# Optimization experiments

Measured on AMD Instinct MI355X. Metric: run time of the kernel, lower is better.

## Reference

```python
import math
import jax, jax.numpy as jnp
import numpy as np

B, L, CIN, COUT = 128, 100, 55, 55
D, H, DFF, MODES = 512, 8, 512, 32
E = D // H
KERNELS = (12, 24)
NK = len(KERNELS)


def _pos_emb(length, d):
    pos = np.arange(length)[:, None].astype(np.float32)
    div = np.exp(np.arange(0, d, 2).astype(np.float32) * (-math.log(10000.0) / d))
    pe = np.zeros((length, d), dtype=np.float32)
    pe[:, 0::2] = np.sin(pos * div)
    pe[:, 1::2] = np.cos(pos * div)
    return jnp.asarray(pe)


def _circ_conv3(x, W):
    # Conv1d(kernel=3, padding=1, padding_mode='circular', bias=False); x:(B,L,C) W:(O,C,3)
    n = x.shape[1]
    xp = jnp.concatenate([x[:, -1:], x, x[:, :1]], axis=1)
    return (jnp.einsum('blc,oc->blo', xp[:, 0:n], W[:, :, 0]) +
            jnp.einsum('blc,oc->blo', xp[:, 1:n + 1], W[:, :, 1]) +
            jnp.einsum('blc,oc->blo', xp[:, 2:n + 2], W[:, :, 2]))


def _moving_avg(x, k):
    # replicate-pad then length-preserving mean filter (Autoformer moving_avg)
    front = jnp.repeat(x[:, :1], (k - 1) // 2, axis=1)
    end = jnp.repeat(x[:, -1:], k // 2, axis=1)
    xp = jnp.concatenate([front, x, end], axis=1)
    c = jnp.cumsum(xp, axis=1)
    c = jnp.concatenate([jnp.zeros_like(c[:, :1]), c], axis=1)
    return (c[:, k:] - c[:, :-k]) / float(k)


def _decomp(x, w, b):
    # series_decomp_multi with learned softmax mixing (Linear(1, NK))
    means = jnp.stack([_moving_avg(x, k) for k in KERNELS], axis=-1)  # (B,L,D,NK)
    mix = jax.nn.softmax(x[..., None] * w + b, axis=-1)
    mean = jnp.sum(means * mix, axis=-1)
    return x - mean, mean


def _my_layernorm(x, g, b):
    mu = x.mean(-1, keepdims=True)
    var = ((x - mu) ** 2).mean(-1, keepdims=True)
    xh = (x - mu) / jnp.sqrt(var + 1e-5) * g + b
    return xh - xh.mean(axis=1, keepdims=True)


def _fourier_block(q, Wc):
    # q:(B,L,H,E) -> rfft over L, per-mode complex GEMM with Wc:(H,E,E,MODES), irfft
    x = jnp.transpose(q, (0, 2, 3, 1))  # (B,H,E,L)
    xf = jnp.fft.rfft(x, axis=-1)
    sel = jnp.einsum('bhem,heom->bhom', xf[..., :MODES], Wc)
    nfreq = x.shape[-1] // 2 + 1
    out_ft = jnp.zeros(sel.shape[:-1] + (nfreq,), sel.dtype).at[..., :MODES].set(sel)
    out = jnp.fft.irfft(out_ft, n=x.shape[-1], axis=-1)
    return jnp.transpose(out, (0, 3, 1, 2))  # (B,L,H,E)


def _fourier_cross(q, k, Wc):
    # FourierCrossAttention: frequency-domain q*k attention with tanh activation, values = k
    xq = jnp.transpose(q, (0, 2, 3, 1))
    xk = jnp.transpose(k, (0, 2, 3, 1))
    qf = jnp.fft.rfft(xq, axis=-1)[..., :MODES]
    kf = jnp.fft.rfft(xk, axis=-1)[..., :MODES]
    qk = jnp.tanh(jnp.einsum('bhex,bhey->bhxy', qf, kf))
    qkv = jnp.einsum('bhxy,bhey->bhex', qk, kf)
    w = jnp.einsum('bhex,heox->bhox', qkv, Wc)
    nfreq = xq.shape[-1] // 2 + 1
    out_ft = jnp.zeros(w.shape[:-1] + (nfreq,), w.dtype).at[..., :MODES].set(w)
    out = jnp.fft.irfft(out_ft / float(D * D), n=xq.shape[-1], axis=-1)
    return jnp.transpose(out, (0, 3, 1, 2))


def _heads(x, W, b):
    y = x @ W.T + b
    return y.reshape(y.shape[0], y.shape[1], H, E)


def _gelu(x):
    return jax.nn.gelu(x, approximate=False)


def _forward(x, emb_enc_w, emb_dec_w, enc_proj_w, enc_proj_b, enc_sig_w, enc_sig_b,
             enc_four_wr, enc_four_wi, enc_ffn_w1, enc_ffn_w2, enc_dcmp_w, enc_dcmp_b,
             enc_norm_g, enc_norm_b, dec_proj_w, dec_proj_b, dec_four_wr, dec_four_wi,
             crs_proj_w, crs_proj_b, crs_four_wr, crs_four_wi, dec_ffn_w1, dec_ffn_w2,
             dec_dcmp_w, dec_dcmp_b, dec_trend_w, dec_norm_g, dec_norm_b,
             out_proj_w, out_proj_b):
    b, n, _ = x.shape
    dist = jnp.abs(jnp.arange(n)[:, None] - jnp.arange(n)[None, :]).astype(x.dtype)
    # seasonal-trend init decomposition
    trend_init = jnp.broadcast_to(x.mean(axis=1, keepdims=True), x.shape)
    seasonal_init = x - trend_init
    pe = _pos_emb(n, D)
    enc_four = enc_four_wr + 1j * enc_four_wi
    enc = _circ_conv3(x, emb_enc_w) + pe
    series_l, prior_l, sigma_l = [], [], []
    for i in range(enc_proj_w.shape[0]):  # e_layers (structurally distinct params)
        Wp, bp = enc_proj_w[i], enc_proj_b[i]
        q = _heads(enc, Wp[0], bp[0])
        k = _heads(enc, Wp[1], bp[1])
        v = _heads(enc, Wp[2], bp[2])  # projected but unused by FourierBlock (faithful)
        attn_out = _fourier_block(q, enc_four).reshape(b, n, D) @ Wp[3].T + bp[3]
        # Anomaly-Transformer association: series = softmax(QK^T/sqrt(E)), prior = Gaussian kernel
        scores = jnp.einsum('blhe,bshe->bhls', q, k) / math.sqrt(E)
        series = jax.nn.softmax(scores, axis=-1)
        sig = jnp.transpose(enc @ enc_sig_w[i].T + enc_sig_b[i], (0, 2, 1))  # (B,H,L)
        sig = jnp.power(3.0, jax.nn.sigmoid(5.0 * sig) + 1e-5) - 1.0
        prior = jnp.exp(-dist ** 2 / (2.0 * sig[..., None] ** 2)) / (math.sqrt(2.0 * math.pi) * sig[..., None])
        series_l.append(series); prior_l.append(prior); sigma_l.append(sig)
        h = enc + attn_out
        h, _ = _decomp(h, enc_dcmp_w[i, 0], enc_dcmp_b[i, 0])
        y = _gelu(h @ enc_ffn_w1[i].T) @ enc_ffn_w2[i].T
        enc, _ = _decomp(h + y, enc_dcmp_w[i, 1], enc_dcmp_b[i, 1])
    enc = _my_layernorm(enc, enc_norm_g, enc_norm_b)

    # decoder (d_layers = 1)
    dec = _circ_conv3(seasonal_init, emb_dec_w) + pe
    dec_four = dec_four_wr + 1j * dec_four_wi
    crs_four = crs_four_wr + 1j * crs_four_wi
    q = _heads(dec, dec_proj_w[0], dec_proj_b[0])
    sa = _fourier_block(q, dec_four).reshape(b, n, D) @ dec_proj_w[3].T + dec_proj_b[3]
    h = dec + sa
    h, t1 = _decomp(h, dec_dcmp_w[0], dec_dcmp_b[0])
    qc = _heads(h, crs_proj_w[0], crs_proj_b[0])
    kc = _heads(enc, crs_proj_w[1], crs_proj_b[1])
    ca = _fourier_cross(qc, kc, crs_four).reshape(b, n, D) @ crs_proj_w[3].T + crs_proj_b[3]
    h = h + ca
    h, t2 = _decomp(h, dec_dcmp_w[1], dec_dcmp_b[1])
    y = _gelu(h @ dec_ffn_w1.T) @ dec_ffn_w2.T
    h, t3 = _decomp(h + y, dec_dcmp_w[2], dec_dcmp_b[2])
    residual_trend = _circ_conv3(t1 + t2 + t3, dec_trend_w)  # (B,L,COUT)
    trend = trend_init + residual_trend
    h = _my_layernorm(h, dec_norm_g, dec_norm_b)
    seasonal = h @ out_proj_w.T + out_proj_b
    dec_out = trend + seasonal
    return dec_out, jnp.stack(series_l), jnp.stack(prior_l), jnp.stack(sigma_l)


def setup_inputs() -> dict:
    key = jax.random.key(0)
    ks = iter(jax.random.split(key, 64))

    def rn(shape, s=0.02):
        return s * jax.random.normal(next(ks), shape, dtype=jnp.float32)

    return dict(
        x=jax.random.normal(next(ks), (B, L, CIN), dtype=jnp.float32),
        emb_enc_w=rn((D, CIN, 3)), emb_dec_w=rn((D, CIN, 3)),
        enc_proj_w=rn((2, 4, D, D)), enc_proj_b=jnp.zeros((2, 4, D), jnp.float32),
        enc_sig_w=rn((2, H, D)), enc_sig_b=jnp.zeros((2, H), jnp.float32),
        enc_four_wr=rn((H, E, E, MODES)), enc_four_wi=rn((H, E, E, MODES)),
        enc_ffn_w1=rn((2, DFF, D)), enc_ffn_w2=rn((2, D, DFF)),
        enc_dcmp_w=rn((2, 2, NK), 1.0), enc_dcmp_b=jnp.zeros((2, 2, NK), jnp.float32),
        enc_norm_g=jnp.ones((D,), jnp.float32), enc_norm_b=jnp.zeros((D,), jnp.float32),
        dec_proj_w=rn((4, D, D)), dec_proj_b=jnp.zeros((4, D), jnp.float32),
        dec_four_wr=rn((H, E, E, MODES)), dec_four_wi=rn((H, E, E, MODES)),
        crs_proj_w=rn((4, D, D)), crs_proj_b=jnp.zeros((4, D), jnp.float32),
        crs_four_wr=rn((H, E, E, MODES)), crs_four_wi=rn((H, E, E, MODES)),
        dec_ffn_w1=rn((DFF, D)), dec_ffn_w2=rn((D, DFF)),
        dec_dcmp_w=rn((3, NK), 1.0), dec_dcmp_b=jnp.zeros((3, NK), jnp.float32),
        dec_trend_w=rn((COUT, D, 3)),
        dec_norm_g=jnp.ones((D,), jnp.float32), dec_norm_b=jnp.zeros((D,), jnp.float32),
        out_proj_w=rn((COUT, D)), out_proj_b=jnp.zeros((COUT,), jnp.float32),
    )


def reference(x, emb_enc_w, emb_dec_w, enc_proj_w, enc_proj_b, enc_sig_w, enc_sig_b,
              enc_four_wr, enc_four_wi, enc_ffn_w1, enc_ffn_w2, enc_dcmp_w, enc_dcmp_b,
              enc_norm_g, enc_norm_b, dec_proj_w, dec_proj_b, dec_four_wr, dec_four_wi,
              crs_proj_w, crs_proj_b, crs_four_wr, crs_four_wi, dec_ffn_w1, dec_ffn_w2,
              dec_dcmp_w, dec_dcmp_b, dec_trend_w, dec_norm_g, dec_norm_b,
              out_proj_w, out_proj_b):
    return _forward(x, emb_enc_w, emb_dec_w, enc_proj_w, enc_proj_b, enc_sig_w, enc_sig_b,
                    enc_four_wr, enc_four_wi, enc_ffn_w1, enc_ffn_w2, enc_dcmp_w, enc_dcmp_b,
                    enc_norm_g, enc_norm_b, dec_proj_w, dec_proj_b, dec_four_wr, dec_four_wi,
                    crs_proj_w, crs_proj_b, crs_four_wr, crs_four_wi, dec_ffn_w1, dec_ffn_w2,
                    dec_dcmp_w, dec_dcmp_b, dec_trend_w, dec_norm_g, dec_norm_b,
                    out_proj_w, out_proj_b)
```

## Files before the change

### kernel.cpp

```cpp
#include <hip/hip_runtime.h>
#include <hip/hip_bf16.h>
#include <cmath>

constexpr int B = 128, L = 100, CIN = 55, COUT = 55;
constexpr int D = 512, H = 8, DFF = 512, MODES = 32, E = 64;
constexpr int NK = 2;
constexpr int M_ROWS = B * L;
constexpr int KEMB = 192;
constexpr size_t BLD  = (size_t)B * L * D;
constexpr size_t BHEM = (size_t)B * H * E * MODES;
constexpr size_t BHLL = (size_t)B * H * L * L;
constexpr float INV_SQRT_2PI = 0.3989422804014327f;

static inline int cdiv(int a, int b) { return (a + b - 1) / b; }

typedef short shortx8 __attribute__((ext_vector_type(8)));
typedef float f32x4 __attribute__((ext_vector_type(4)));

__device__ inline unsigned short f2bf(float f)
{
    unsigned int u = __float_as_uint(f);
    unsigned int r = (u + 0x7FFFu + ((u >> 16) & 1u)) >> 16;
    return (unsigned short)r;
}
__device__ inline unsigned short f2bf_n(float f)
{
    union { __hip_bfloat16 h; unsigned short u; } cv;
    cv.h = __float2bfloat16(f);
    return cv.u;
}
__device__ inline float bf2f(unsigned short u)
{
    union { unsigned int i; float f; } c;
    c.i = (unsigned int)u << 16;
    return c.f;
}

__global__ void init_consts(float* __restrict__ pe)
{
    int idx = blockIdx.x * 256 + threadIdx.x;
    if (idx < L * D) {
        int l = idx / D, d = idx % D;
        int i2 = d & ~1;
        float div = expf((float)i2 * (-logf(10000.f) / (float)D));
        float ang = (float)l * div;
        pe[idx] = (d & 1) ? cosf(ang) : sinf(ang);
    }
}

__global__ void init_tw(unsigned short* __restrict__ twf, unsigned short* __restrict__ twi)
{
    int idx = blockIdx.x * 256 + threadIdx.x;
    if (idx >= 64 * 128) return;
    {
        int mp = idx / 128, t = idx % 128;
        float v = 0.f;
        if (t < L) {
            if (mp < 32) v = cosf(2.f * 3.14159265358979323846f * (float)mp * (float)t / (float)L);
            else v = -sinf(2.f * 3.14159265358979323846f * (float)(mp - 32) * (float)t / (float)L);
        }
        twf[idx] = f2bf(v);
    }
    {
        int t = idx / 64, mp = idx % 64;
        float v = 0.f;
        if (t < L) {
            if (mp == 0) v = 1.f;
            else if (mp < 32) v = 2.f * cosf(2.f * 3.14159265358979323846f * (float)mp * (float)t / (float)L);
            else if (mp == 32) v = 0.f;
            else v = -2.f * sinf(2.f * 3.14159265358979323846f * (float)(mp - 32) * (float)t / (float)L);
        }
        twi[idx] = f2bf(v);
    }
}

__global__ void xmean_kernel(const float* __restrict__ x, float* __restrict__ xm)
{
    int idx = blockIdx.x * 256 + threadIdx.x;
    if (idx >= B * CIN) return;
    int b = idx / CIN, c = idx % CIN;
    float s = 0.f;
    for (int l = 0; l < L; ++l) s += x[((size_t)b * L + l) * CIN + c];
    xm[idx] = s * (1.f / (float)L);
}

__global__ void to_bf16(const float* __restrict__ src, unsigned short* __restrict__ dst, int n4)
{
    int i = blockIdx.x * 256 + threadIdx.x;
    if (i >= n4) return;
    float4 v = *(const float4*)&src[(size_t)i * 4];
    ushort4 h;
    h.x = f2bf(v.x); h.y = f2bf(v.y); h.z = f2bf(v.z); h.w = f2bf(v.w);
    *(ushort4*)&dst[(size_t)i * 4] = h;
}

__global__ void pad_rows_bf(const float* __restrict__ src, unsigned short* __restrict__ dst,
                            int rows_src, int rows_dst, int k_src, int k_dst)
{
    int idx = blockIdx.x * 256 + threadIdx.x;
    if (idx >= rows_dst * k_dst) return;
    int r = idx / k_dst, k = idx % k_dst;
    dst[idx] = (r < rows_src && k < k_src) ? f2bf(src[(size_t)r * k_src + k]) : (unsigned short)0;
}

__global__ void pad_trend_w2_bf(const float* __restrict__ src, unsigned short* __restrict__ dst)
{
    int idx = blockIdx.x * 256 + threadIdx.x;
    if (idx >= 192 * D) return;
    int n = idx / D, d = idx % D;
    int j = n / 64, o = n % 64;
    dst[idx] = (o < COUT) ? f2bf(src[(size_t)o * (D * 3) + d * 3 + j]) : (unsigned short)0;
}

__global__ __launch_bounds__(256) void transpose_w(const float* __restrict__ wr, const float* __restrict__ wi,
                                                   float2* __restrict__ wt)
{
    int h = blockIdx.x / E, e = blockIdx.x % E;
    __shared__ float tr[64][33], ti[64][33];
    for (int i = threadIdx.x; i < E * MODES; i += 256) {
        int o = i / MODES, m = i % MODES;
        size_t s = (((size_t)h * E + e) * E + o) * MODES + m;
        tr[o][m] = wr[s]; ti[o][m] = wi[s];
    }
    __syncthreads();
    for (int i = threadIdx.x; i < MODES * E; i += 256) {
        int m = i / E, o = i % E;
        wt[(((size_t)h * MODES + m) * E + e) * E + o] = make_float2(tr[o][m], ti[o][m]);
    }
}

__global__ void im2col_emb(const float* __restrict__ x, const float* __restrict__ xmean,
                           unsigned short* __restrict__ A2)
{
    int idx = blockIdx.x * 256 + threadIdx.x;
    if (idx >= M_ROWS * KEMB) return;
    int k = idx % KEMB, m = idx / KEMB;
    float v = 0.f;
    if (k < CIN * 3) {
        int c = k / 3, j = k % 3;
        int l = m % L, b = m / L;
        int ls = l + j - 1; ls = (ls + L) % L;
        v = x[((size_t)b * L + ls) * CIN + c];
        if (xmean) v -= xmean[(size_t)b * CIN + c];
    }
    A2[idx] = f2bf(v);
}

template<int BN>
__global__ __launch_bounds__(256) void gemm_mfma(const unsigned short* __restrict__ A,
                                                 const unsigned short* __restrict__ Wb,
                                                 const float* __restrict__ bias, const float* __restrict__ pe,
                                                 float* __restrict__ C, unsigned short* __restrict__ Cb,
                                                 int Nout, int K, int act, int accum)
{
    constexpr int NI = BN / 32;
    constexpr int BI = BN / 64;
    __shared__ unsigned short As[2][128][40];
    __shared__ unsigned short Bs[2][BN][40];
    int tid = threadIdx.x;
    int row0 = blockIdx.y * 128, col0 = blockIdx.x * BN;
    int wid = tid >> 6, lane = tid & 63;
    int wm = wid >> 1, wn = wid & 1;
    int lrow = lane & 15, kg = lane >> 4;
    int ar = tid >> 2, ac8 = (tid & 3) * 8;
    f32x4 acc[4][NI] = {};
    shortx8 rah[2], rbh[BI];

    auto loadG = [&](int k0) {
#pragma unroll
        for (int p = 0; p < 2; ++p)
            rah[p] = *(const shortx8*)&A[(size_t)(row0 + p * 64 + ar) * K + k0 + ac8];
#pragma unroll
        for (int p = 0; p < BI; ++p)
            rbh[p] = *(const shortx8*)&Wb[(size_t)(col0 + p * 64 + ar) * K + k0 + ac8];
    };
    auto storeLDS = [&](int buf) {
#pragma unroll
        for (int p = 0; p < 2; ++p)
            *(shortx8*)&As[buf][p * 64 + ar][ac8] = rah[p];
#pragma unroll
        for (int p = 0; p < BI; ++p)
            *(shortx8*)&Bs[buf][p * 64 + ar][ac8] = rbh[p];
    };

    int nk = K >> 5;
    loadG(0);
    storeLDS(0);
    if (nk > 1) loadG(32);
    __syncthreads();
    int cur = 0;
    for (int s = 0; s < nk; ++s) {
        if (s + 1 < nk) {
            storeLDS(cur ^ 1);
            if (s + 2 < nk) loadG((s + 2) << 5);
        }
        shortx8 av[4], bv[NI];
#pragma unroll
        for (int mi = 0; mi < 4; ++mi)
            av[mi] = *(const shortx8*)&As[cur][wm * 64 + mi * 16 + lrow][kg * 8];
#pragma unroll
        for (int ni = 0; ni < NI; ++ni)
            bv[ni] = *(const shortx8*)&Bs[cur][wn * (BN / 2) + ni * 16 + lrow][kg * 8];
#pragma unroll
        for (int mi = 0; mi < 4; ++mi)
#pragma unroll
            for (int ni = 0; ni < NI; ++ni)
                acc[mi][ni] = __builtin_amdgcn_mfma_f32_16x16x32_bf16(av[mi], bv[ni], acc[mi][ni], 0, 0, 0);
        if (s + 1 < nk) __syncthreads();
        cur ^= 1;
    }
#pragma unroll
    for (int mi = 0; mi < 4; ++mi) {
#pragma unroll
        for (int ni = 0; ni < NI; ++ni) {
            int col = col0 + wn * (BN / 2) + ni * 16 + lrow;
            if (col >= Nout) continue;
#pragma unroll
            for (int r = 0; r < 4; ++r) {
                int row = row0 + wm * 64 + mi * 16 + kg * 4 + r;
                float v = acc[mi][ni][r];
                if (bias) v += bias[col];
                if (pe) v += pe[(size_t)(row % L) * Nout + col];
                if (act) v = 0.5f * v * (1.f + erff(v * 0.70710678118654752f));
                size_t o = (size_t)row * Nout + col;
                if (Cb) Cb[o] = f2bf_n(v);
                else if (accum) C[o] += v;
                else C[o] = v;
            }
        }
    }
}

__global__ __launch_bounds__(256) void scores_softmax(const unsigned short* __restrict__ QK,
                                                      float* __restrict__ out)
{
    int bh = blockIdx.x, b = bh / H, h = bh % H;
    int pass = blockIdx.y;
    __shared__ unsigned short Ks[112][72];
    __shared__ unsigned short Qs[64][72];
    int tid = threadIdx.x;
    int srow = tid >> 4, sc4 = (tid & 15) * 4;
#pragma unroll
    for (int i = 0; i < 7; ++i) {
        int r = i * 16 + srow;
        ushort4 hh = {0, 0, 0, 0};
        if (r < L) hh = *(const ushort4*)&QK[((size_t)b * L + r) * 1024 + 512 + h * E + sc4];
        *(ushort4*)&Ks[r][sc4] = hh;
    }
#pragma unroll
    for (int i = 0; i < 4; ++i) {
        int r = i * 16 + srow;
        int gr = pass * 64 + r;
        ushort4 hh = {0, 0, 0, 0};
        if (gr < L) hh = *(const ushort4*)&QK[((size_t)b * L + gr) * 1024 + h * E + sc4];
        *(ushort4*)&Qs[r][sc4] = hh;
    }
    __syncthreads();
    int wid = tid >> 6, lane = tid & 63;
    int lrow = lane & 15, kg = lane >> 4;
    f32x4 acc[7] = {};
#pragma unroll
    for (int ks = 0; ks < 2; ++ks) {
        shortx8 aq = *(const shortx8*)&Qs[wid * 16 + lrow][ks * 32 + kg * 8];
#pragma unroll
        for (int tj = 0; tj < 7; ++tj) {
            shortx8 bk = *(const shortx8*)&Ks[tj * 16 + lrow][ks * 32 + kg * 8];
            acc[tj] = __builtin_amdgcn_mfma_f32_16x16x32_bf16(aq, bk, acc[tj], 0, 0, 0);
        }
    }
    float mx[4] = {-1e30f, -1e30f, -1e30f, -1e30f};
#pragma unroll
    for (int tj = 0; tj < 7; ++tj) {
        bool valid = (tj * 16 + lrow) < L;
#pragma unroll
        for (int r = 0; r < 4; ++r) {
            float v = acc[tj][r] * 0.125f;
            acc[tj][r] = valid ? v : -1e30f;
            if (valid) mx[r] = fmaxf(mx[r], v);
        }
    }
#pragma unroll
    for (int off = 1; off < 16; off <<= 1)
#pragma unroll
        for (int r = 0; r < 4; ++r) mx[r] = fmaxf(mx[r], __shfl_xor(mx[r], off));
    float sum[4] = {0.f, 0.f, 0.f, 0.f};
#pragma unroll
    for (int tj = 0; tj < 7; ++tj)
#pragma unroll
        for (int r = 0; r < 4; ++r) {
            float e = expf(acc[tj][r] - mx[r]);
            acc[tj][r] = e;
            sum[r] += e;
        }
#pragma unroll
    for (int off = 1; off < 16; off <<= 1)
#pragma unroll
        for (int r = 0; r < 4; ++r) sum[r] += __shfl_xor(sum[r], off);
    float inv[4];
#pragma unroll
    for (int r = 0; r < 4; ++r) inv[r] = 1.f / sum[r];
    float* base = out + (size_t)bh * L * L;
#pragma unroll
    for (int r = 0; r < 4; ++r) {
        int row = pass * 64 + wid * 16 + kg * 4 + r;
        if (row >= L) continue;
#pragma unroll
        for (int tj = 0; tj < 7; ++tj) {
            int col = tj * 16 + lrow;
            if (col < L) base[(size_t)row * L + col] = acc[tj][r] * inv[r];
        }
    }
}

__global__ void trend_combine(const float* __restrict__ Y, const float* __restrict__ xmean,
                              float* __restrict__ dec_out)
{
    int idx = blockIdx.x * 256 + threadIdx.x;
    if (idx >= B * L * COUT) return;
    int o = idx % COUT; int l = (idx / COUT) % L; int b = idx / (COUT * L);
    int lm = (l + L - 1) % L, lp = (l + 1) % L;
    float v = xmean[(size_t)b * CIN + o]
            + Y[((size_t)b * L + lm) * 192 + o]
            + Y[((size_t)b * L + l ) * 192 + 64 + o]
            + Y[((size_t)b * L + lp) * 192 + 128 + o];
    dec_out[idx] = v;
}

__global__ __launch_bounds__(256) void dft_mfma(const unsigned short* __restrict__ X,
                                                const unsigned short* __restrict__ twf,
                                                float2* __restrict__ xf, int stride)
{
    int b = blockIdx.x / H, h = blockIdx.x % H;
    __shared__ unsigned short Xs[64][136];
    int tid = threadIdx.x;
    for (int i = tid; i < L * E / 4; i += 256) {
        int t = i >> 4, e4 = (i & 15) * 4;
        ushort4 u = *(const ushort4*)&X[((size_t)b * L + t) * stride + h * E + e4];
        Xs[e4][t] = u.x; Xs[e4 + 1][t] = u.y; Xs[e4 + 2][t] = u.z; Xs[e4 + 3][t] = u.w;
    }
    for (int i = tid; i < 64 * 28; i += 256) {
        int e = i / 28, t = L + i % 28;
        Xs[e][t] = 0;
    }
    __syncthreads();
    int wid = tid >> 6, lane = tid & 63;
    int lrow = lane & 15, kg = lane >> 4;
    f32x4 acc[4] = {};
#pragma unroll
    for (int k0 = 0; k0 < 4; ++k0) {
        shortx8 bx = *(const shortx8*)&Xs[wid * 16 + lrow][k0 * 32 + kg * 8];
#pragma unroll
        for (int mi = 0; mi < 4; ++mi) {
            shortx8 aw = *(const shortx8*)&twf[(size_t)(mi * 16 + lrow) * 128 + k0 * 32 + kg * 8];
            acc[mi] = __builtin_amdgcn_mfma_f32_16x16x32_bf16(aw, bx, acc[mi], 0, 0, 0);
        }
    }
    int e = wid * 16 + lrow;
#pragma unroll
    for (int mi = 0; mi < 2; ++mi)
#pragma unroll
        for (int r = 0; r < 4; ++r) {
            int m = mi * 16 + kg * 4 + r;
            xf[((size_t)(h * MODES + m) * B + b) * E + e] = make_float2(acc[mi][r], acc[mi + 2][r]);
        }
}

__global__ __launch_bounds__(256) void idft_mfma(const float2* __restrict__ sel,
                                                 const unsigned short* __restrict__ twi,
                                                 unsigned short* __restrict__ out, float scale)
{
    int b = blockIdx.x / H, h = blockIdx.x % H;
    __shared__ unsigned short Ss[64][72];
    int tid = threadIdx.x;
    for (int i = tid; i < MODES * E; i += 256) {
        int m = i >> 6, o = i & 63;
        float2 v = sel[((size_t)(h * MODES + m) * B + b) * E + o];
        Ss[o][m] = f2bf_n(v.x);
        Ss[o][m + 32] = f2bf_n(v.y);
    }
    __syncthreads();
    int wid = tid >> 6, lane = tid & 63;
    int lrow = lane & 15, kg = lane >> 4;
    f32x4 acc[2][4] = {};
#pragma unroll
    for (int k0 = 0; k0 < 2; ++k0) {
        shortx8 bs[4];
#pragma unroll
        for (int ni = 0; ni < 4; ++ni)
            bs[ni] = *(const shortx8*)&Ss[ni * 16 + lrow][k0 * 32 + kg * 8];
#pragma unroll
        for (int ti = 0; ti < 2; ++ti) {
            shortx8 at = *(const shortx8*)&twi[(size_t)((wid * 2 + ti) * 16 + lrow) * 64 + k0 * 32 + kg * 8];
#pragma unroll
            for (int ni = 0; ni < 4; ++ni)
                acc[ti][ni] = __builtin_amdgcn_mfma_f32_16x16x32_bf16(at, bs[ni], acc[ti][ni], 0, 0, 0);
        }
    }
#pragma unroll
    for (int ti = 0; ti < 2; ++ti)
#pragma unroll
        for (int ni = 0; ni < 4; ++ni)
#pragma unroll
            for (int r = 0; r < 4; ++r) {
                int t = (wid * 2 + ti) * 16 + kg * 4 + r;
                if (t < L) {
                    int o = ni * 16 + lrow;
                    out[((size_t)b * L + t) * D + h * E + o] = f2bf_n(acc[ti][ni][r] * scale);
                }
            }
}

__global__ __launch_bounds__(256) void mode_gemm2(float2* __restrict__ xf, const float2* __restrict__ wt)
{
    int hm = blockIdx.x;
    int bt = blockIdx.y;
    __shared__ float2 Wc[E][E];
    __shared__ float2 Ac[32][E];
    for (int i = threadIdx.x; i < E * E; i += 256) Wc[i / E][i % E] = wt[(size_t)hm * (E * E) + i];
    for (int i = threadIdx.x; i < 32 * E; i += 256)
        Ac[i / E][i % E] = xf[((size_t)hm * B + bt * 32 + i / E) * E + i % E];
    __syncthreads();
    int o = threadIdx.x & 63, bb = threadIdx.x >> 6;
    float2 acc[8];
#pragma unroll
    for (int j = 0; j < 8; ++j) acc[j] = make_float2(0.f, 0.f);
    for (int e = 0; e < E; ++e) {
        float2 w = Wc[e][o];
#pragma unroll
        for (int j = 0; j < 8; ++j) {
            float2 a = Ac[bb * 8 + j][e];
            acc[j].x += a.x * w.x - a.y * w.y;
            acc[j].y += a.x * w.y + a.y * w.x;
        }
    }
#pragma unroll
    for (int j = 0; j < 8; ++j)
        xf[((size_t)hm * B + bt * 32 + bb * 8 + j) * E + o] = acc[j];
}

__global__ __launch_bounds__(256) void fourier_qk(const float2* __restrict__ qf, float2* __restrict__ kf)
{
    int b = blockIdx.x / H, h = blockIdx.x % H;
    __shared__ float2 qm[MODES][E + 1], km[MODES][E + 1], vm[MODES][E + 1];
    __shared__ float tr[MODES][MODES + 1], ti[MODES][MODES + 1];
    for (int i = threadIdx.x; i < MODES * E; i += 256) {
        int m = i / E, e = i % E;
        size_t idx = ((size_t)(h * MODES + m) * B + b) * E + e;
        qm[m][e] = qf[idx];
        km[m][e] = kf[idx];
    }
    __syncthreads();
    for (int i = threadIdx.x; i < MODES * MODES; i += 256) {
        int x = i / MODES, y = i % MODES;
        float re = 0.f, im = 0.f;
        for (int e = 0; e < E; ++e) {
            float2 a = qm[x][e], k2 = km[y][e];
            re += a.x * k2.x - a.y * k2.y;
            im += a.x * k2.y + a.y * k2.x;
        }
        float aa = fminf(fmaxf(2.f * re, -30.f), 30.f);
        float b2 = 2.f * im;
        float den = coshf(aa) + cosf(b2);
        tr[x][y] = sinhf(aa) / den;
        ti[x][y] = sinf(b2) / den;
    }
    __syncthreads();
    for (int i = threadIdx.x; i < MODES * E; i += 256) {
        int x = i / E, e = i % E;
        float re = 0.f, im = 0.f;
        for (int y = 0; y < MODES; ++y) {
            float ar = tr[x][y], ai = ti[x][y];
            float2 kk = km[y][e];
            re += ar * kk.x - ai * kk.y;
            im += ar * kk.y + ai * kk.x;
        }
        vm[x][e] = make_float2(re, im);
    }
    __syncthreads();
    for (int i = threadIdx.x; i < MODES * E; i += 256) {
        int m = i / E, e = i % E;
        kf[((size_t)(h * MODES + m) * B + b) * E + e] = vm[m][e];
    }
}

__global__ __launch_bounds__(256) void sigma_prior(const unsigned short* __restrict__ enc,
                                                   const float* __restrict__ w,
                                                   const float* __restrict__ bias,
                                                   float* __restrict__ sig_out, float* __restrict__ prior)
{
    __shared__ float wsh[H][D];
    for (int i = threadIdx.x; i < H * D; i += 256) wsh[i / D][i % D] = w[i];
    __syncthreads();
    int wid = threadIdx.x / 64, lane = threadIdx.x % 64;
    int row = blockIdx.x * 4 + wid;
    const unsigned short* p = enc + (size_t)row * D;
    float xv[8];
#pragma unroll
    for (int i = 0; i < 8; ++i) xv[i] = bf2f(p[lane + i * 64]);
    int b = row / L, l = row % L;
#pragma unroll
    for (int h = 0; h < H; ++h) {
        float s = 0.f;
#pragma unroll
        for (int i = 0; i < 8; ++i) s += xv[i] * wsh[h][lane + i * 64];
        for (int off = 32; off; off >>= 1) s += __shfl_xor(s, off);
        float acc = s + bias[h];
        float sg = 1.f / (1.f + expf(-5.f * acc));
        float val = expf((sg + 1e-5f) * 1.0986122886681098f) - 1.f;
        if (lane == 0) sig_out[((size_t)b * H + h) * L + l] = val;
        float inv2 = 1.f / (2.f * val * val);
        float coef = INV_SQRT_2PI / val;
        float* pr = prior + (((size_t)b * H + h) * L + l) * L;
        for (int sc = lane; sc < L; sc += 64) {
            float d = (float)abs(l - sc);
            pr[sc] = expf(-d * d * inv2) * coef;
        }
    }
}

__global__ __launch_bounds__(256) void decomp_kernel(const unsigned short* __restrict__ in1,
                                                     const unsigned short* __restrict__ in2,
                                                     const float* __restrict__ w, const float* __restrict__ bc,
                                                     unsigned short* __restrict__ res, float* __restrict__ trend,
                                                     unsigned short* __restrict__ trend16, int tmode)
{
    int b = blockIdx.x / (D / 64);
    int d0 = (blockIdx.x % (D / 64)) * 64;
    __shared__ float P[125][65];
    __shared__ float qtot[4][64];
    int tid = threadIdx.x;
    int dd = tid & 63, q = tid >> 6;
    int p0 = q * 31;
    float run = 0.f;
#pragma unroll
    for (int i = 0; i < 31; ++i) {
        int p = p0 + i;
        int j = min(max(p - 12, 0), L - 1);
        size_t g = ((size_t)b * L + j) * D + d0 + dd;
        float v = bf2f(in1[g]);
        if (in2) v += bf2f(in2[g]);
        run += v;
        P[p + 1][dd] = run;
    }
    qtot[q][dd] = run;
    if (tid < 64) P[0][dd] = 0.f;
    __syncthreads();
    if (q > 0) {
        float off = qtot[0][dd];
        if (q > 1) off += qtot[1][dd];
        if (q > 2) off += qtot[2][dd];
#pragma unroll
        for (int i = 0; i < 31; ++i)
            P[p0 + i + 1][dd] += off;
    }
    __syncthreads();
    float w0 = w[0], w1 = w[1], b0 = bc[0], b1 = bc[1];
    for (int i = tid; i < L * 64; i += 256) {
        int l = i >> 6, d2 = i & 63;
        float s12 = P[l + 19][d2] - P[l + 7][d2];
        float s24 = P[l + 25][d2] - P[l + 1][d2];
        float x = P[l + 13][d2] - P[l + 12][d2];
        float m0 = s12 * (1.f / 12.f), m1 = s24 * (1.f / 24.f);
        float z0 = x * w0 + b0, z1 = x * w1 + b1;
        float zm = fmaxf(z0, z1);
        float e0 = expf(z0 - zm), e1 = expf(z1 - zm);
        float p0f = e0 / (e0 + e1);
        float mean = m0 * p0f + m1 * (1.f - p0f);
        size_t g = ((size_t)b * L + l) * D + d0 + d2;
        res[g] = f2bf_n(x - mean);
        if (tmode == 1) trend[g] = mean;
        else if (tmode == 2) {
            float tv = trend[g] + mean;
            trend[g] = tv;
            if (trend16) trend16[g] = f2bf_n(tv);
        }
    }
}

__global__ __launch_bounds__(256) void ln_colsub(const unsigned short* __restrict__ x,
                                                 const float* __restrict__ g, const float* __restrict__ bb,
                                                 unsigned short* __restrict__ out)
{
    int b = blockIdx.x;
    __shared__ unsigned short xs[L][D];
    __shared__ float colmean[D];
    __shared__ float gs[D], bs2[D];
    int tid = threadIdx.x;
    for (int i = tid; i < L * D / 8; i += 256) {
        int l = i / 64, c8 = (i % 64) * 8;
        *(shortx8*)&xs[l][c8] = *(const shortx8*)&x[((size_t)b * L + l) * D + c8];
    }
    for (int i = tid; i < D; i += 256) { gs[i] = g[i]; bs2[i] = bb[i]; }
    __syncthreads();
    int wid = tid >> 6, lane = tid & 63;
    for (int l = wid; l < L; l += 4) {
        float v[8];
        float s = 0.f, s2 = 0.f;
#pragma unroll
        for (int i = 0; i < 8; ++i) {
            v[i] = bf2f(xs[l][lane + i * 64]);
            s += v[i]; s2 += v[i] * v[i];
        }
        for (int off = 32; off; off >>= 1) { s += __shfl_xor(s, off); s2 += __shfl_xor(s2, off); }
        float mu = s / (float)D;
        float var = s2 / (float)D - mu * mu;
        float rstd = rsqrtf(var + 1e-5f);
#pragma unroll
        for (int i = 0; i < 8; ++i) {
            int d = lane + i * 64;
            xs[l][d] = f2bf_n((v[i] - mu) * rstd * gs[d] + bs2[d]);
        }
    }
    __syncthreads();
    for (int c = tid; c < D; c += 256) {
        float s = 0.f;
        for (int l = 0; l < L; ++l) s += bf2f(xs[l][c]);
        colmean[c] = s * (1.f / (float)L);
    }
    __syncthreads();
    for (int i = tid; i < L * D; i += 256) {
        int l = i / D, c = i % D;
        out[((size_t)b * L + l) * D + c] = f2bf_n(bf2f(xs[l][c]) - colmean[c]);
    }
}

extern "C" void kernel_launch(void* const* d_in, const int* in_sizes, int n_in,
                              void* d_out, int out_size, void* d_ws, size_t ws_size,
                              hipStream_t stream)
{
    const float* x           = (const float*)d_in[0];
    const float* emb_enc_w   = (const float*)d_in[1];
    const float* emb_dec_w   = (const float*)d_in[2];
    const float* enc_proj_w  = (const float*)d_in[3];
    const float* enc_proj_b  = (const float*)d_in[4];
    const float* enc_sig_w   = (const float*)d_in[5];
    const float* enc_sig_b   = (const float*)d_in[6];
    const float* enc_four_wr = (const float*)d_in[7];
    const float* enc_four_wi = (const float*)d_in[8];
    const float* enc_ffn_w1  = (const float*)d_in[9];
    const float* enc_ffn_w2  = (const float*)d_in[10];
    const float* enc_dcmp_w  = (const float*)d_in[11];
    const float* enc_dcmp_b  = (const float*)d_in[12];
    const float* enc_norm_g  = (const float*)d_in[13];
    const float* enc_norm_b  = (const float*)d_in[14];
    const float* dec_proj_w  = (const float*)d_in[15];
    const float* dec_proj_b  = (const float*)d_in[16];
    const float* dec_four_wr = (const float*)d_in[17];
    const float* dec_four_wi = (const float*)d_in[18];
    const float* crs_proj_w  = (const float*)d_in[19];
    const float* crs_proj_b  = (const float*)d_in[20];
    const float* crs_four_wr = (const float*)d_in[21];
    const float* crs_four_wi = (const float*)d_in[22];
    const float* dec_ffn_w1  = (const float*)d_in[23];
    const float* dec_ffn_w2  = (const float*)d_in[24];
    const float* dec_dcmp_w  = (const float*)d_in[25];
    const float* dec_dcmp_b  = (const float*)d_in[26];
    const float* dec_trend_w = (const float*)d_in[27];
    const float* dec_norm_g  = (const float*)d_in[28];
    const float* dec_norm_b  = (const float*)d_in[29];
    const float* out_proj_w  = (const float*)d_in[30];
    const float* out_proj_b  = (const float*)d_in[31];

    float* ws = (float*)d_ws;
    size_t off = 0;
    float* pe    = ws + off; off += (size_t)L * D;
    float* xmean = ws + off; off += (size_t)B * CIN;
    float* bufF  = ws + off; off += BLD;
    float* tacc  = ws + off; off += BLD;
    float2* xfc  = (float2*)(ws + off); off += 2 * BHEM;
    float2* kfc  = (float2*)(ws + off); off += 2 * BHEM;
    float2* wtb  = (float2*)(ws + off); off += 2 * (size_t)H * MODES * E * E;
    unsigned short* qk16 = (unsigned short*)(ws + off); off += BLD;
    unsigned short* e16  = (unsigned short*)(ws + off); off += BLD / 2;
    unsigned short* c16  = (unsigned short*)(ws + off); off += BLD / 2;
    unsigned short* d16  = (unsigned short*)(ws + off); off += BLD / 2;
    unsigned short* h16  = (unsigned short*)(ws + off); off += BLD / 2;
    unsigned short* t16  = (unsigned short*)(ws + off); off += BLD / 2;
    unsigned short* im16 = (unsigned short*)(ws + off); off += (size_t)M_ROWS * KEMB / 2;
    unsigned short* wbf_encproj = (unsigned short*)(ws + off); off += (size_t)2 * 4 * D * D / 2;
    unsigned short* wbf_ffn1    = (unsigned short*)(ws + off); off += (size_t)2 * DFF * D / 2;
    unsigned short* wbf_ffn2    = (unsigned short*)(ws + off); off += (size_t)2 * D * DFF / 2;
    unsigned short* wbf_decproj = (unsigned short*)(ws + off); off += (size_t)4 * D * D / 2;
    unsigned short* wbf_crsproj = (unsigned short*)(ws + off); off += (size_t)4 * D * D / 2;
    unsigned short* wbf_dffn1   = (unsigned short*)(ws + off); off += (size_t)DFF * D / 2;
    unsigned short* wbf_dffn2   = (unsigned short*)(ws + off); off += (size_t)D * DFF / 2;
    unsigned short* wbf_embenc  = (unsigned short*)(ws + off); off += (size_t)D * KEMB / 2;
    unsigned short* wbf_embdec  = (unsigned short*)(ws + off); off += (size_t)D * KEMB / 2;
    unsigned short* wbf_trd     = (unsigned short*)(ws + off); off += (size_t)192 * D / 2;
    unsigned short* wbf_seas    = (unsigned short*)(ws + off); off += (size_t)64 * D / 2;
    unsigned short* twf         = (unsigned short*)(ws + off); off += (size_t)64 * 128 / 2;
    unsigned short* twi         = (unsigned short*)(ws + off); off += (size_t)128 * 64 / 2;
    unsigned short* a16 = qk16;
    unsigned short* b16 = qk16 + BLD;

    float* out       = (float*)d_out;
    float* dec_out   = out;
    float* series_out= out + (size_t)B * L * COUT;
    float* prior_out = series_out + 2 * BHLL;
    float* sigma_out = prior_out + 2 * BHLL;

    const int BH = B * H;

    init_consts<<<200, 256, 0, stream>>>(pe);
    init_tw<<<32, 256, 0, stream>>>(twf, twi);
    xmean_kernel<<<cdiv(B * CIN, 256), 256, 0, stream>>>(x, xmean);
    to_bf16<<<cdiv(2 * 4 * D * D / 4, 256), 256, 0, stream>>>(enc_proj_w, wbf_encproj, 2 * 4 * D * D / 4);
    to_bf16<<<cdiv(2 * DFF * D / 4, 256), 256, 0, stream>>>(enc_ffn_w1, wbf_ffn1, 2 * DFF * D / 4);
    to_bf16<<<cdiv(2 * D * DFF / 4, 256), 256, 0, stream>>>(enc_ffn_w2, wbf_ffn2, 2 * D * DFF / 4);
    to_bf16<<<cdiv(4 * D * D / 4, 256), 256, 0, stream>>>(dec_proj_w, wbf_decproj, 4 * D * D / 4);
    to_bf16<<<cdiv(4 * D * D / 4, 256), 256, 0, stream>>>(crs_proj_w, wbf_crsproj, 4 * D * D / 4);
    to_bf16<<<cdiv(DFF * D / 4, 256), 256, 0, stream>>>(dec_ffn_w1, wbf_dffn1, DFF * D / 4);
    to_bf16<<<cdiv(D * DFF / 4, 256), 256, 0, stream>>>(dec_ffn_w2, wbf_dffn2, D * DFF / 4);
    pad_rows_bf<<<cdiv(D * KEMB, 256), 256, 0, stream>>>(emb_enc_w, wbf_embenc, D, D, CIN * 3, KEMB);
    pad_rows_bf<<<cdiv(D * KEMB, 256), 256, 0, stream>>>(emb_dec_w, wbf_embdec, D, D, CIN * 3, KEMB);
    pad_trend_w2_bf<<<cdiv(192 * D, 256), 256, 0, stream>>>(dec_trend_w, wbf_trd);
    pad_rows_bf<<<cdiv(64 * D, 256), 256, 0, stream>>>(out_proj_w, wbf_seas, COUT, 64, D, D);
    transpose_w<<<H * E, 256, 0, stream>>>(enc_four_wr, enc_four_wi, wtb);

    auto gemm = [&](const unsigned short* A, const unsigned short* Wb, const float* bias, const float* pe_,
                    float* C, unsigned short* Cb, int N, int Nout, int K, int act, int accum) {
        if (N % 128 == 0) {
            dim3 grid(N / 128, M_ROWS / 128);
            gemm_mfma<128><<<grid, 256, 0, stream>>>(A, Wb, bias, pe_, C, Cb, Nout, K, act, accum);
        } else {
            dim3 grid(N / 64, M_ROWS / 128);
            gemm_mfma<64><<<grid, 256, 0, stream>>>(A, Wb, bias, pe_, C, Cb, Nout, K, act, accum);
        }
    };
    dim3 mg_grid(H * MODES, B / 32);
    dim3 sc_grid(BH, 2);

    im2col_emb<<<cdiv(M_ROWS * KEMB, 256), 256, 0, stream>>>(x, nullptr, im16);
    gemm(im16, wbf_embenc, nullptr, pe, nullptr, e16, D, D, KEMB, 0, 0);

    for (int i = 0; i < 2; ++i) {
        const unsigned short* Wp = wbf_encproj + (size_t)i * 4 * D * D;
        const float* bp = enc_proj_b + (size_t)i * 4 * D;
        float* series_i = series_out + (size_t)i * BHLL;
        float* prior_i  = prior_out  + (size_t)i * BHLL;
        float* sigma_i  = sigma_out  + (size_t)i * B * H * L;

        gemm(e16, Wp, bp, nullptr, nullptr, qk16, 1024, 1024, D, 0, 0);
        dft_mfma<<<BH, 256, 0, stream>>>(qk16, twf, xfc, 1024);
        mode_gemm2<<<mg_grid, 256, 0, stream>>>(xfc, wtb);
        idft_mfma<<<BH, 256, 0, stream>>>(xfc, twi, c16, 1.f / (float)L);
        gemm(c16, Wp + (size_t)3 * D * D, bp + 3 * D, nullptr, nullptr, d16, D, D, D, 0, 0);
        scores_softmax<<<sc_grid, 256, 0, stream>>>(qk16, series_i);
        sigma_prior<<<M_ROWS / 4, 256, 0, stream>>>(e16, enc_sig_w + (size_t)i * H * D,
                                                    enc_sig_b + (size_t)i * H, sigma_i, prior_i);
        decomp_kernel<<<B * (D / 64), 256, 0, stream>>>(e16, d16, enc_dcmp_w + (size_t)(i * 2 + 0) * NK,
                                                        enc_dcmp_b + (size_t)(i * 2 + 0) * NK, h16, nullptr, nullptr, 0);
        gemm(h16, wbf_ffn1 + (size_t)i * DFF * D, nullptr, nullptr, nullptr, c16, DFF, DFF, D, 1, 0);
        gemm(c16, wbf_ffn2 + (size_t)i * D * DFF, nullptr, nullptr, nullptr, d16, D, D, DFF, 0, 0);
        decomp_kernel<<<B * (D / 64), 256, 0, stream>>>(h16, d16, enc_dcmp_w + (size_t)(i * 2 + 1) * NK,
                                                        enc_dcmp_b + (size_t)(i * 2 + 1) * NK, e16, nullptr, nullptr, 0);
    }
    ln_colsub<<<B, 256, 0, stream>>>(e16, enc_norm_g, enc_norm_b, e16);

    transpose_w<<<H * E, 256, 0, stream>>>(dec_four_wr, dec_four_wi, wtb);
    im2col_emb<<<cdiv(M_ROWS * KEMB, 256), 256, 0, stream>>>(x, xmean, im16);
    gemm(im16, wbf_embdec, nullptr, pe, nullptr, a16, D, D, KEMB, 0, 0);
    gemm(a16, wbf_decproj, dec_proj_b, nullptr, nullptr, b16, D, D, D, 0, 0);
    dft_mfma<<<BH, 256, 0, stream>>>(b16, twf, xfc, D);
    mode_gemm2<<<mg_grid, 256, 0, stream>>>(xfc, wtb);
    idft_mfma<<<BH, 256, 0, stream>>>(xfc, twi, c16, 1.f / (float)L);
    gemm(c16, wbf_decproj + (size_t)3 * D * D, dec_proj_b + 3 * D, nullptr, nullptr, d16, D, D, D, 0, 0);
    decomp_kernel<<<B * (D / 64), 256, 0, stream>>>(a16, d16, dec_dcmp_w, dec_dcmp_b, h16, tacc, nullptr, 1);

    gemm(h16, wbf_crsproj, crs_proj_b, nullptr, nullptr, b16, D, D, D, 0, 0);
    dft_mfma<<<BH, 256, 0, stream>>>(b16, twf, xfc, D);
    gemm(e16, wbf_crsproj + (size_t)D * D, crs_proj_b + D, nullptr, nullptr, b16, D, D, D, 0, 0);
    dft_mfma<<<BH, 256, 0, stream>>>(b16, twf, kfc, D);
    transpose_w<<<H * E, 256, 0, stream>>>(crs_four_wr, crs_four_wi, wtb);
    fourier_qk<<<BH, 256, 0, stream>>>(xfc, kfc);
    mode_gemm2<<<mg_grid, 256, 0, stream>>>(kfc, wtb);
    idft_mfma<<<BH, 256, 0, stream>>>(kfc, twi, c16, 1.f / ((float)L * (float)D * (float)D));
    gemm(c16, wbf_crsproj + (size_t)3 * D * D, crs_proj_b + 3 * D, nullptr, nullptr, d16, D, D, D, 0, 0);
    decomp_kernel<<<B * (D / 64), 256, 0, stream>>>(h16, d16, dec_dcmp_w + NK, dec_dcmp_b + NK, a16, tacc, nullptr, 2);

    gemm(a16, wbf_dffn1, nullptr, nullptr, nullptr, c16, DFF, DFF, D, 1, 0);
    gemm(c16, wbf_dffn2, nullptr, nullptr, nullptr, d16, D, D, DFF, 0, 0);
    decomp_kernel<<<B * (D / 64), 256, 0, stream>>>(a16, d16, dec_dcmp_w + 2 * NK, dec_dcmp_b + 2 * NK, b16, tacc, t16, 2);

    gemm(t16, wbf_trd, nullptr, nullptr, bufF, nullptr, 192, 192, D, 0, 0);
    trend_combine<<<cdiv(B * L * COUT, 256), 256, 0, stream>>>(bufF, xmean, dec_out);

    ln_colsub<<<B, 256, 0, stream>>>(b16, dec_norm_g, dec_norm_b, d16);
    gemm(d16, wbf_seas, out_proj_b, nullptr, dec_out, nullptr, 64, COUT, D, 0, 1);
}
```

Before: 1.303 ms.

## Load GEMM MFMA fragments directly from global memory, removing LDS staging

The bf16 MFMA GEMM no longer stages tiles in shared memory. Each wave now loads its own A and B fragments straight from global memory into registers, double-buffered in registers, and drops all __syncthreads. This removes LDS traffic and barrier stalls. In exchange, operand reuse across the block's waves is lost, so global and L2 traffic rise, and each load is only 16 bytes per lane across strided rows.

```diff
diff --git a/kernel.cpp b/kernel.cpp
--- a/kernel.cpp
+++ b/kernel.cpp
@@ -154,70 +154,64 @@
                                                  int Nout, int K, int act, int accum)
 {
     constexpr int NI = BN / 32;
-    constexpr int BI = BN / 64;
-    __shared__ unsigned short As[2][128][40];
-    __shared__ unsigned short Bs[2][BN][40];
     int tid = threadIdx.x;
-    int row0 = blockIdx.y * 128, col0 = blockIdx.x * BN;
     int wid = tid >> 6, lane = tid & 63;
     int wm = wid >> 1, wn = wid & 1;
     int lrow = lane & 15, kg = lane >> 4;
-    int ar = tid >> 2, ac8 = (tid & 3) * 8;
+    int row0 = blockIdx.y * 128 + wm * 64;
+    int col0 = blockIdx.x * BN + wn * (BN / 2);
+    const unsigned short* pA = A + (size_t)(row0 + lrow) * K + kg * 8;
+    const unsigned short* pB = Wb + (size_t)(col0 + lrow) * K + kg * 8;
     f32x4 acc[4][NI] = {};
-    shortx8 rah[2], rbh[BI];
-
-    auto loadG = [&](int k0) {
-#pragma unroll
-        for (int p = 0; p < 2; ++p)
-            rah[p] = *(const shortx8*)&A[(size_t)(row0 + p * 64 + ar) * K + k0 + ac8];
-#pragma unroll
-        for (int p = 0; p < BI; ++p)
-            rbh[p] = *(const shortx8*)&Wb[(size_t)(col0 + p * 64 + ar) * K + k0 + ac8];
+    shortx8 a0[4], b0[NI], a1[4], b1[NI];
+
+    auto load0 = [&](int k0) {
+#pragma unroll
+        for (int mi = 0; mi < 4; ++mi) a0[mi] = *(const shortx8*)&pA[(size_t)mi * 16 * K + k0];
+#pragma unroll
+        for (int ni = 0; ni < NI; ++ni) b0[ni] = *(const shortx8*)&pB[(size_t)ni * 16 * K + k0];
     };
-    auto storeLDS = [&](int buf) {
-#pragma unroll
-        for (int p = 0; p < 2; ++p)
-            *(shortx8*)&As[buf][p * 64 + ar][ac8] = rah[p];
-#pragma unroll
-        for (int p = 0; p < BI; ++p)
-            *(shortx8*)&Bs[buf][p * 64 + ar][ac8] = rbh[p];
+    auto load1 = [&](int k0) {
+#pragma unroll
+        for (int mi = 0; mi < 4; ++mi) a1[mi] = *(const shortx8*)&pA[(size_t)mi * 16 * K + k0];
+#pragma unroll
+        for (int ni = 0; ni < NI; ++ni) b1[ni] = *(const shortx8*)&pB[(size_t)ni * 16 * K + k0];
     };
+    auto mfma0 = [&]() {
+#pragma unroll
+        for (int mi = 0; mi < 4; ++mi)
+#pragma unroll
+            for (int ni = 0; ni < NI; ++ni)
+                acc[mi][ni] = __builtin_amdgcn_mfma_f32_16x16x32_bf16(a0[mi], b0[ni], acc[mi][ni], 0, 0, 0);
+    };
+    auto mfma1 = [&]() {
+#pragma unroll
+        for (int mi = 0; mi < 4; ++mi)
+#pragma unroll
+            for (int ni = 0; ni < NI; ++ni)
+                acc[mi][ni] = __builtin_amdgcn_mfma_f32_16x16x32_bf16(a1[mi], b1[ni], acc[mi][ni], 0, 0, 0);
+    };
 
     int nk = K >> 5;
-    loadG(0);
-    storeLDS(0);
-    if (nk > 1) loadG(32);
-    __syncthreads();
-    int cur = 0;
-    for (int s = 0; s < nk; ++s) {
-        if (s + 1 < nk) {
-            storeLDS(cur ^ 1);
-            if (s + 2 < nk) loadG((s + 2) << 5);
-        }
-        shortx8 av[4], bv[NI];
-#pragma unroll
-        for (int mi = 0; mi < 4; ++mi)
-            av[mi] = *(const shortx8*)&As[cur][wm * 64 + mi * 16 + lrow][kg * 8];
-#pragma unroll
-        for (int ni = 0; ni < NI; ++ni)
-            bv[ni] = *(const shortx8*)&Bs[cur][wn * (BN / 2) + ni * 16 + lrow][kg * 8];
-#pragma unroll
-        for (int mi = 0; mi < 4; ++mi)
-#pragma unroll
-            for (int ni = 0; ni < NI; ++ni)
-                acc[mi][ni] = __builtin_amdgcn_mfma_f32_16x16x32_bf16(av[mi], bv[ni], acc[mi][ni], 0, 0, 0);
-        if (s + 1 < nk) __syncthreads();
-        cur ^= 1;
+    load0(0);
+    int s = 0;
+    while (true) {
+        if (s + 1 < nk) load1((s + 1) << 5);
+        mfma0();
+        if (++s >= nk) break;
+        if (s + 1 < nk) load0((s + 1) << 5);
+        mfma1();
+        if (++s >= nk) break;
     }
 #pragma unroll
     for (int mi = 0; mi < 4; ++mi) {
 #pragma unroll
         for (int ni = 0; ni < NI; ++ni) {
-            int col = col0 + wn * (BN / 2) + ni * 16 + lrow;
+            int col = col0 + ni * 16 + lrow;
             if (col >= Nout) continue;
 #pragma unroll
             for (int r = 0; r < 4; ++r) {
-                int row = row0 + wm * 64 + mi * 16 + kg * 4 + r;
+                int row = row0 + mi * 16 + kg * 4 + r;
                 float v = acc[mi][ni][r];
                 if (bias) v += bias[col];
                 if (pe) v += pe[(size_t)(row % L) * Nout + col];
```

After: 1.615 ms. +23.9%, slower.
